# Optimization experiments

Measured on AMD Instinct MI355X. Metric: run time of the kernel, lower is better.

## Reference

```python
import jax, jax.numpy as jnp
import numpy as np

HIDDEN = 1024
HEADS = 16
HEAD_DIM = HIDDEN // HEADS
SCALE = float(np.sqrt(HEAD_DIM))


def setup_inputs() -> dict:
    key = jax.random.key(0)
    ks = jax.random.split(key, 9)
    B, S = 4, 8192
    std = 1.0 / np.sqrt(HIDDEN)
    x = jax.random.normal(ks[0], (B, S, HIDDEN), dtype=jnp.float32)
    Wq = jax.random.normal(ks[1], (HIDDEN, HIDDEN), dtype=jnp.float32) * std
    Wk = jax.random.normal(ks[2], (HIDDEN, HIDDEN), dtype=jnp.float32) * std
    Wv = jax.random.normal(ks[3], (HIDDEN, HIDDEN), dtype=jnp.float32) * std
    Wo = jax.random.normal(ks[4], (HIDDEN, HIDDEN), dtype=jnp.float32) * std
    bq = jax.random.normal(ks[5], (HIDDEN,), dtype=jnp.float32) * std
    bk = jax.random.normal(ks[6], (HIDDEN,), dtype=jnp.float32) * std
    bv = jax.random.normal(ks[7], (HIDDEN,), dtype=jnp.float32) * std
    bo = jax.random.normal(ks[8], (HIDDEN,), dtype=jnp.float32) * std
    return {"x": x, "Wq": Wq, "bq": bq, "Wk": Wk, "bk": bk,
            "Wv": Wv, "bv": bv, "Wo": Wo, "bo": bo}


def reference(x, Wq, bq, Wk, bk, Wv, bv, Wo, bo):
    B, S, E = x.shape
    H, D = HEADS, HEAD_DIM
    # torch nn.Linear: y = x @ W^T + b
    q = (jnp.einsum('bse,fe->bsf', x, Wq) + bq).reshape(B, S, H, D)
    k = (jnp.einsum('bse,fe->bsf', x, Wk) + bk).reshape(B, S, H, D)
    v = (jnp.einsum('bse,fe->bsf', x, Wv) + bv).reshape(B, S, H, D)
    # Faithful to source: NO head transpose, so matmul contracts over head_dim
    # with (B,S) as batch dims -> per-token head-mixing scores [B,S,H,H].
    scores = jnp.einsum('bshd,bsgd->bshg', q, k) / SCALE
    probs = jax.nn.softmax(scores, axis=-1)
    attn = jnp.einsum('bshg,bsgd->bshd', probs, v).reshape(B, S, E)
    return jnp.einsum('bse,fe->bsf', attn, Wo) + bo
```

## Files before the change

kernel.cpp:

```cpp
#include <hip/hip_runtime.h>
#include <hip/hip_bf16.h>
#include <cstdint>
#include <type_traits>

#define GLOBAL_AS __attribute__((address_space(1)))
#define LDS_AS    __attribute__((address_space(3)))

typedef short bf16x8 __attribute__((ext_vector_type(8)));
typedef short short8_t __attribute__((ext_vector_type(8)));
typedef float f32x4  __attribute__((ext_vector_type(4)));

static constexpr int E_DIM = 1024;
static constexpr int HD = 64;
static constexpr int QKV_STRIDE = 3072;
static constexpr int KDIM = 1024;
static constexpr int NTK  = KDIM / 64;
static constexpr int NIT  = NTK / 2;

__device__ __forceinline__ float b2f(short s) {
    union { unsigned u; float f; } x;
    x.u = ((unsigned)(unsigned short)s) << 16;
    return x.f;
}
__device__ __forceinline__ short f2b(float f) {
    union { float f; unsigned u; } x; x.f = f;
    unsigned r = x.u + 0x7FFF + ((x.u >> 16) & 1);
    return (short)(r >> 16);
}

__global__ __launch_bounds__(256) void k_prep(
    const float* __restrict__ x,
    const float* __restrict__ Wq, const float* __restrict__ Wk,
    const float* __restrict__ Wv, const float* __restrict__ Wo,
    const float* __restrict__ bq, const float* __restrict__ bk,
    const float* __restrict__ bv,
    short* __restrict__ xb, short* __restrict__ Wqkvb, short* __restrict__ Wob,
    float* __restrict__ bqkv, int n4x, int n4w)
{
    int i = blockIdx.x * 256 + threadIdx.x;
    const float* src;
    short* dst;
    int j;
    if (i < n4x)                       { src = x;  dst = xb;                  j = i; }
    else if (i < n4x + n4w)            { src = Wq; dst = Wqkvb;               j = i - n4x; }
    else if (i < n4x + 2 * n4w)        { src = Wk; dst = Wqkvb + 4 * n4w;     j = i - n4x - n4w; }
    else if (i < n4x + 3 * n4w)        { src = Wv; dst = Wqkvb + 8 * n4w;     j = i - n4x - 2 * n4w; }
    else if (i < n4x + 4 * n4w)        { src = Wo; dst = Wob;                 j = i - n4x - 3 * n4w; }
    else {
        int b = i - (n4x + 4 * n4w);
        if (b < 768) {
            #pragma unroll
            for (int e = 0; e < 4; ++e) {
                int idx = b * 4 + e;
                float v = (idx < 1024) ? bq[idx] : (idx < 2048 ? bk[idx - 1024] : bv[idx - 2048]);
                bqkv[idx] = v;
            }
        }
        return;
    }
    float4 v = reinterpret_cast<const float4*>(src)[j];
    short4 o;
    o.x = f2b(v.x); o.y = f2b(v.y); o.z = f2b(v.z); o.w = f2b(v.w);
    reinterpret_cast<short4*>(dst)[j] = o;
}

template <typename OutT>
__global__ __launch_bounds__(512, 2) void k_gemm256(
    const short* __restrict__ A,
    const short* __restrict__ Bm,
    const float* __restrict__ bias,
    OutT* __restrict__ C,
    int NT_N, int N)
{
    __shared__ short lds[65536];

    const int tid  = threadIdx.x;
    const int lane = tid & 63;
    const int wv   = tid >> 6;
    const int wr   = wv >> 2;
    const int wc   = wv & 3;
    const int frow = lane & 15;
    const int ks   = lane >> 4;
    const int sw   = frow & 7;
    const int sl0  = ((0 + ks) ^ sw) * 8;
    const int sl1  = ((4 + ks) ^ sw) * 8;

    const int nwg = gridDim.x, nper = nwg >> 3, bid = blockIdx.x;
    const int swz = (bid & 7) * nper + (bid >> 3);
    const int m0  = (swz / NT_N) * 256;
    const int n0  = (swz % NT_N) * 256;

    const int ArdBase = wr * 8192;
    const int BrdBase = 16384 + (wc >> 1) * 8192 + (wc & 1) * 4096;

    const int srow = tid >> 3;
    const int ssl  = ((tid & 7) ^ (srow & 7)) * 8;
    const int sdst = tid * 8;

#define GLD(SRC, DST) __builtin_amdgcn_global_load_lds(                            \
        (const GLOBAL_AS short*)(SRC), (LDS_AS short*)(DST), 16, 0, 0)
#define STAGE_A(BUF, HALF, T) do {                                                 \
    const short* s_ = A + (size_t)(m0 + (HALF) * 128 + srow) * KDIM + (T) * 64 + ssl; \
    short* d_ = &lds[(BUF) * 32768 + (HALF) * 8192 + sdst];                        \
    GLD(s_, d_);  GLD(s_ + (size_t)64 * KDIM, d_ + 4096);                          \
} while (0)
#define STAGE_B(BUF, HALF, T) do {                                                 \
    const short* s_ = Bm + (size_t)(n0 + (HALF) * 128 + srow) * KDIM + (T) * 64 + ssl; \
    short* d_ = &lds[(BUF) * 32768 + 16384 + (HALF) * 8192 + sdst];                \
    GLD(s_, d_);  GLD(s_ + (size_t)64 * KDIM, d_ + 4096);                          \
} while (0)

#define RD_A(BUF, MIB) do {                                                        \
    _Pragma("unroll")                                                              \
    for (int m_ = 0; m_ < 4; ++m_) {                                               \
        const short* p_ = &lds[(BUF) * 32768 + ArdBase + ((MIB) + m_) * 1024 + frow * 64]; \
        af[m_][0] = *(const bf16x8*)(p_ + sl0);                                    \
        af[m_][1] = *(const bf16x8*)(p_ + sl1);                                    \
    }                                                                              \
} while (0)
#define RD_B(BUF, NIB, BF) do {                                                    \
    _Pragma("unroll")                                                              \
    for (int n_ = 0; n_ < 2; ++n_) {                                               \
        const short* p_ = &lds[(BUF) * 32768 + BrdBase + ((NIB) + n_) * 1024 + frow * 64]; \
        BF[n_][0] = *(const bf16x8*)(p_ + sl0);                                    \
        BF[n_][1] = *(const bf16x8*)(p_ + sl1);                                    \
    }                                                                              \
} while (0)

#define MM2(MB) do {                                                               \
    __builtin_amdgcn_s_setprio(1);                                                 \
    _Pragma("unroll")                                                              \
    for (int m_ = 0; m_ < 4; ++m_) {                                               \
        _Pragma("unroll")                                                          \
        for (int n_ = 0; n_ < 2; ++n_) {                                           \
            acc[(MB)+m_][n_] = __builtin_amdgcn_mfma_f32_16x16x32_bf16(            \
                af[m_][0], bfA[n_][0], acc[(MB)+m_][n_], 0, 0, 0);                 \
            acc[(MB)+m_][n_] = __builtin_amdgcn_mfma_f32_16x16x32_bf16(            \
                af[m_][1], bfA[n_][1], acc[(MB)+m_][n_], 0, 0, 0);                 \
            acc[(MB)+m_][2+n_] = __builtin_amdgcn_mfma_f32_16x16x32_bf16(          \
                af[m_][0], bfB[n_][0], acc[(MB)+m_][2+n_], 0, 0, 0);               \
            acc[(MB)+m_][2+n_] = __builtin_amdgcn_mfma_f32_16x16x32_bf16(          \
                af[m_][1], bfB[n_][1], acc[(MB)+m_][2+n_], 0, 0, 0);               \
        }                                                                          \
    }                                                                              \
    __builtin_amdgcn_s_setprio(0);                                                 \
} while (0)

#define BAR   __builtin_amdgcn_s_barrier()
#define VM4   asm volatile("s_waitcnt vmcnt(4)" ::: "memory")
#define VM8   asm volatile("s_waitcnt vmcnt(8)" ::: "memory")

    f32x4 acc[8][4];
    #pragma unroll
    for (int i = 0; i < 8; ++i)
        #pragma unroll
        for (int j = 0; j < 4; ++j)
            acc[i][j] = (f32x4){0.f, 0.f, 0.f, 0.f};

    bf16x8 af[4][2], bfA[2][2], bfB[2][2];

    STAGE_A(0, 0, 0);  STAGE_A(0, 1, 0);  STAGE_B(0, 0, 0);  STAGE_B(0, 1, 0);
    STAGE_A(1, 0, 1);  STAGE_A(1, 1, 1);  STAGE_B(1, 0, 1);  STAGE_B(1, 1, 1);
    VM8;  BAR;
    RD_A(0, 0);  RD_B(0, 0, bfA);  RD_B(0, 2, bfB);

    #pragma unroll 1
    for (int it = 0; it < NIT; ++it) {
        const int tb = (2 * it + 2 <= 15) ? 2 * it + 2 : 15;
        const int tc = (2 * it + 3 <= 15) ? 2 * it + 3 : 15;

        BAR;
        MM2(0);
        RD_A(0, 4);
        STAGE_B(0, 0, tb);  STAGE_B(0, 1, tb);
        VM4;
        BAR;
        MM2(4);
        STAGE_A(0, 0, tb);  STAGE_A(0, 1, tb);
        RD_A(1, 0);  RD_B(1, 0, bfA);  RD_B(1, 2, bfB);
        BAR;
        MM2(0);
        RD_A(1, 4);
        STAGE_B(1, 0, tc);  STAGE_B(1, 1, tc);
        VM4;
        BAR;
        MM2(4);
        STAGE_A(1, 0, tc);  STAGE_A(1, 1, tc);
        RD_A(0, 0);  RD_B(0, 0, bfA);  RD_B(0, 2, bfB);
    }

    asm volatile("s_waitcnt vmcnt(0)" ::: "memory");

    const int crow = (lane >> 4) * 4;
    const int ccol = lane & 15;
    float bv4[4];
    #pragma unroll
    for (int ni = 0; ni < 4; ++ni)
        bv4[ni] = bias[n0 + wc * 64 + ni * 16 + ccol];
    #pragma unroll
    for (int mi = 0; mi < 8; ++mi) {
        #pragma unroll
        for (int r = 0; r < 4; ++r) {
            const size_t rowg = (size_t)(m0 + wr * 128 + mi * 16 + crow + r) * N;
            #pragma unroll
            for (int ni = 0; ni < 4; ++ni) {
                const int col = n0 + wc * 64 + ni * 16 + ccol;
                float v = acc[mi][ni][r] + bv4[ni];
                if constexpr (std::is_same<OutT, float>::value) {
                    C[rowg + col] = v;
                } else {
                    C[rowg + col] = f2b(v);
                }
            }
        }
    }
#undef GLD
#undef STAGE_A
#undef STAGE_B
#undef RD_A
#undef RD_B
#undef MM2
#undef BAR
#undef VM4
#undef VM8
}

__global__ __launch_bounds__(256) void k_attn(
    const short* __restrict__ QKV, short* __restrict__ O)
{
    __shared__ short Ks[16][1032];
    __shared__ short Vs[16][1032];

    const int tid = threadIdx.x;
    const int tok0 = blockIdx.x * 16;

    for (int i = tid; i < 2048; i += 256) {
        int t = i >> 7;
        int j = i & 127;
        const size_t base = (size_t)(tok0 + t) * QKV_STRIDE;
        *reinterpret_cast<short8_t*>(&Ks[t][j * 8]) =
            *reinterpret_cast<const short8_t*>(&QKV[base + 1024 + j * 8]);
        *reinterpret_cast<short8_t*>(&Vs[t][j * 8]) =
            *reinterpret_cast<const short8_t*>(&QKV[base + 2048 + j * 8]);
    }
    __syncthreads();

    const int tl = tid >> 4;
    const int h  = tid & 15;

    float qf[64];
    const short* qp = QKV + (size_t)(tok0 + tl) * QKV_STRIDE + h * HD;
    #pragma unroll
    for (int i = 0; i < 8; ++i) {
        short8_t v = *reinterpret_cast<const short8_t*>(&qp[i * 8]);
        #pragma unroll
        for (int j = 0; j < 8; ++j) qf[i * 8 + j] = b2f(v[j]);
    }

    float s[16];
    #pragma unroll
    for (int g = 0; g < 16; ++g) {
        float a = 0.f;
        #pragma unroll
        for (int i = 0; i < 8; ++i) {
            short8_t kv = *reinterpret_cast<const short8_t*>(&Ks[tl][g * HD + i * 8]);
            #pragma unroll
            for (int j = 0; j < 8; ++j) a += qf[i * 8 + j] * b2f(kv[j]);
        }
        s[g] = a * 0.125f;
    }
    float mx = s[0];
    #pragma unroll
    for (int g = 1; g < 16; ++g) mx = fmaxf(mx, s[g]);
    float l = 0.f;
    #pragma unroll
    for (int g = 0; g < 16; ++g) { s[g] = __expf(s[g] - mx); l += s[g]; }
    const float inv = 1.f / l;
    #pragma unroll
    for (int g = 0; g < 16; ++g) s[g] *= inv;

    short* op = O + (size_t)(tok0 + tl) * E_DIM + h * HD;
    #pragma unroll
    for (int c = 0; c < 4; ++c) {
        float a[16];
        #pragma unroll
        for (int j = 0; j < 16; ++j) a[j] = 0.f;
        #pragma unroll
        for (int g = 0; g < 16; ++g) {
            short8_t v0 = *reinterpret_cast<const short8_t*>(&Vs[tl][g * HD + c * 16]);
            short8_t v1 = *reinterpret_cast<const short8_t*>(&Vs[tl][g * HD + c * 16 + 8]);
            #pragma unroll
            for (int j = 0; j < 8; ++j) {
                a[j]     += s[g] * b2f(v0[j]);
                a[8 + j] += s[g] * b2f(v1[j]);
            }
        }
        short8_t o0, o1;
        #pragma unroll
        for (int j = 0; j < 8; ++j) { o0[j] = f2b(a[j]); o1[j] = f2b(a[8 + j]); }
        *reinterpret_cast<short8_t*>(&op[c * 16])     = o0;
        *reinterpret_cast<short8_t*>(&op[c * 16 + 8]) = o1;
    }
}

extern "C" void kernel_launch(void* const* d_in, const int* in_sizes, int n_in,
                              void* d_out, int out_size, void* d_ws, size_t ws_size,
                              hipStream_t stream) {
    const float* x  = (const float*)d_in[0];
    const float* Wq = (const float*)d_in[1];
    const float* bq = (const float*)d_in[2];
    const float* Wk = (const float*)d_in[3];
    const float* bk = (const float*)d_in[4];
    const float* Wv = (const float*)d_in[5];
    const float* bv = (const float*)d_in[6];
    const float* Wo = (const float*)d_in[7];
    const float* bo = (const float*)d_in[8];
    float* out = (float*)d_out;

    const int T = in_sizes[0] / E_DIM;
    char* ws = (char*)d_ws;
    const size_t SZ_X    = (size_t)T * E_DIM * 2;
    const size_t SZ_WQKV = (size_t)3 * E_DIM * E_DIM * 2;
    const size_t SZ_W    = (size_t)E_DIM * E_DIM * 2;
    const size_t SZ_B    = 3072 * sizeof(float) + 4096;

    short* xb    = (short*)(ws);
    short* Wqkvb = (short*)(ws + SZ_X);
    short* Wob   = (short*)(ws + SZ_X + SZ_WQKV);
    float* bqkv  = (float*)(ws + SZ_X + SZ_WQKV + SZ_W);
    short* QKVb  = (short*)(ws + SZ_X + SZ_WQKV + SZ_W + SZ_B);
    short* Ab    = xb;

    const int n4x = T * E_DIM / 4;
    const int n4w = E_DIM * E_DIM / 4;
    const int nprep = n4x + 4 * n4w + 768;
    k_prep<<<dim3((nprep + 255) / 256), dim3(256), 0, stream>>>(
        x, Wq, Wk, Wv, Wo, bq, bk, bv, xb, Wqkvb, Wob, bqkv, n4x, n4w);

    k_gemm256<short><<<dim3((T / 256) * (QKV_STRIDE / 256)), dim3(512), 0, stream>>>(
        xb, Wqkvb, bqkv, QKVb, QKV_STRIDE / 256, QKV_STRIDE);

    k_attn<<<dim3(T / 16), dim3(256), 0, stream>>>(QKVb, Ab);

    k_gemm256<float><<<dim3((T / 256) * (E_DIM / 256)), dim3(512), 0, stream>>>(
        Ab, Wob, bo, out, E_DIM / 256, E_DIM);
}
```

Before: 393.5 us.

## Use 4-wave 256x256 GEMM blocks with 128x128 per-wave tiles

The GEMM kernel drops from 8 waves to 4 waves per 256x256 block, so each wave computes a 128x128 output tile with 8x8 MFMA accumulators. Global-to-LDS staging issues four loads per thread instead of two, and the wait counts are doubled to match. Each wave now reuses more data per LDS read and there are fewer waves to synchronise, but accumulator register pressure rises sharply (256 floats), which could limit occupancy or cause spills, and there is less latency hiding.

```diff
diff --git a/kernel.cpp b/kernel.cpp
--- a/kernel.cpp
+++ b/kernel.cpp
@@ -65,7 +65,7 @@
 }
 
 template <typename OutT>
-__global__ __launch_bounds__(512, 2) void k_gemm256(
+__global__ __launch_bounds__(256, 1) void k_gemm256(
     const short* __restrict__ A,
     const short* __restrict__ Bm,
     const float* __restrict__ bias,
@@ -77,8 +77,8 @@
     const int tid  = threadIdx.x;
     const int lane = tid & 63;
     const int wv   = tid >> 6;
-    const int wr   = wv >> 2;
-    const int wc   = wv & 3;
+    const int wr   = wv >> 1;
+    const int wc   = wv & 1;
     const int frow = lane & 15;
     const int ks   = lane >> 4;
     const int sw   = frow & 7;
@@ -91,23 +91,26 @@
     const int n0  = (swz % NT_N) * 256;
 
     const int ArdBase = wr * 8192;
-    const int BrdBase = 16384 + (wc >> 1) * 8192 + (wc & 1) * 4096;
+    const int BrdBase = 16384 + wc * 8192;
 
     const int srow = tid >> 3;
     const int ssl  = ((tid & 7) ^ (srow & 7)) * 8;
-    const int sdst = tid * 8;
 
 #define GLD(SRC, DST) __builtin_amdgcn_global_load_lds(                            \
         (const GLOBAL_AS short*)(SRC), (LDS_AS short*)(DST), 16, 0, 0)
 #define STAGE_A(BUF, HALF, T) do {                                                 \
-    const short* s_ = A + (size_t)(m0 + (HALF) * 128 + srow) * KDIM + (T) * 64 + ssl; \
-    short* d_ = &lds[(BUF) * 32768 + (HALF) * 8192 + sdst];                        \
-    GLD(s_, d_);  GLD(s_ + (size_t)64 * KDIM, d_ + 4096);                          \
+    _Pragma("unroll")                                                              \
+    for (int q_ = 0; q_ < 4; ++q_) {                                               \
+        GLD(A + (size_t)(m0 + (HALF) * 128 + srow + 32 * q_) * KDIM + (T) * 64 + ssl, \
+            &lds[(BUF) * 32768 + (HALF) * 8192 + (tid + 256 * q_) * 8]);           \
+    }                                                                              \
 } while (0)
 #define STAGE_B(BUF, HALF, T) do {                                                 \
-    const short* s_ = Bm + (size_t)(n0 + (HALF) * 128 + srow) * KDIM + (T) * 64 + ssl; \
-    short* d_ = &lds[(BUF) * 32768 + 16384 + (HALF) * 8192 + sdst];                \
-    GLD(s_, d_);  GLD(s_ + (size_t)64 * KDIM, d_ + 4096);                          \
+    _Pragma("unroll")                                                              \
+    for (int q_ = 0; q_ < 4; ++q_) {                                               \
+        GLD(Bm + (size_t)(n0 + (HALF) * 128 + srow + 32 * q_) * KDIM + (T) * 64 + ssl, \
+            &lds[(BUF) * 32768 + 16384 + (HALF) * 8192 + (tid + 256 * q_) * 8]);   \
+    }                                                                              \
 } while (0)
 
 #define RD_A(BUF, MIB) do {                                                        \
@@ -120,7 +123,7 @@
 } while (0)
 #define RD_B(BUF, NIB, BF) do {                                                    \
     _Pragma("unroll")                                                              \
-    for (int n_ = 0; n_ < 2; ++n_) {                                               \
+    for (int n_ = 0; n_ < 4; ++n_) {                                               \
         const short* p_ = &lds[(BUF) * 32768 + BrdBase + ((NIB) + n_) * 1024 + frow * 64]; \
         BF[n_][0] = *(const bf16x8*)(p_ + sl0);                                    \
         BF[n_][1] = *(const bf16x8*)(p_ + sl1);                                    \
@@ -132,37 +135,37 @@
     _Pragma("unroll")                                                              \
     for (int m_ = 0; m_ < 4; ++m_) {                                               \
         _Pragma("unroll")                                                          \
-        for (int n_ = 0; n_ < 2; ++n_) {                                           \
+        for (int n_ = 0; n_ < 4; ++n_) {                                           \
             acc[(MB)+m_][n_] = __builtin_amdgcn_mfma_f32_16x16x32_bf16(            \
                 af[m_][0], bfA[n_][0], acc[(MB)+m_][n_], 0, 0, 0);                 \
             acc[(MB)+m_][n_] = __builtin_amdgcn_mfma_f32_16x16x32_bf16(            \
                 af[m_][1], bfA[n_][1], acc[(MB)+m_][n_], 0, 0, 0);                 \
-            acc[(MB)+m_][2+n_] = __builtin_amdgcn_mfma_f32_16x16x32_bf16(          \
-                af[m_][0], bfB[n_][0], acc[(MB)+m_][2+n_], 0, 0, 0);               \
-            acc[(MB)+m_][2+n_] = __builtin_amdgcn_mfma_f32_16x16x32_bf16(          \
-                af[m_][1], bfB[n_][1], acc[(MB)+m_][2+n_], 0, 0, 0);               \
+            acc[(MB)+m_][4+n_] = __builtin_amdgcn_mfma_f32_16x16x32_bf16(          \
+                af[m_][0], bfB[n_][0], acc[(MB)+m_][4+n_], 0, 0, 0);               \
+            acc[(MB)+m_][4+n_] = __builtin_amdgcn_mfma_f32_16x16x32_bf16(          \
+                af[m_][1], bfB[n_][1], acc[(MB)+m_][4+n_], 0, 0, 0);               \
         }                                                                          \
     }                                                                              \
     __builtin_amdgcn_s_setprio(0);                                                 \
 } while (0)
 
 #define BAR   __builtin_amdgcn_s_barrier()
-#define VM4   asm volatile("s_waitcnt vmcnt(4)" ::: "memory")
 #define VM8   asm volatile("s_waitcnt vmcnt(8)" ::: "memory")
-
-    f32x4 acc[8][4];
+#define VM16  asm volatile("s_waitcnt vmcnt(16)" ::: "memory")
+
+    f32x4 acc[8][8];
     #pragma unroll
     for (int i = 0; i < 8; ++i)
         #pragma unroll
-        for (int j = 0; j < 4; ++j)
+        for (int j = 0; j < 8; ++j)
             acc[i][j] = (f32x4){0.f, 0.f, 0.f, 0.f};
 
-    bf16x8 af[4][2], bfA[2][2], bfB[2][2];
+    bf16x8 af[4][2], bfA[4][2], bfB[4][2];
 
     STAGE_A(0, 0, 0);  STAGE_A(0, 1, 0);  STAGE_B(0, 0, 0);  STAGE_B(0, 1, 0);
     STAGE_A(1, 0, 1);  STAGE_A(1, 1, 1);  STAGE_B(1, 0, 1);  STAGE_B(1, 1, 1);
-    VM8;  BAR;
-    RD_A(0, 0);  RD_B(0, 0, bfA);  RD_B(0, 2, bfB);
+    VM16;  BAR;
+    RD_A(0, 0);  RD_B(0, 0, bfA);  RD_B(0, 4, bfB);
 
     #pragma unroll 1
     for (int it = 0; it < NIT; ++it) {
@@ -173,39 +176,39 @@
         MM2(0);
         RD_A(0, 4);
         STAGE_B(0, 0, tb);  STAGE_B(0, 1, tb);
-        VM4;
+        VM8;
         BAR;
         MM2(4);
         STAGE_A(0, 0, tb);  STAGE_A(0, 1, tb);
-        RD_A(1, 0);  RD_B(1, 0, bfA);  RD_B(1, 2, bfB);
+        RD_A(1, 0);  RD_B(1, 0, bfA);  RD_B(1, 4, bfB);
         BAR;
         MM2(0);
         RD_A(1, 4);
         STAGE_B(1, 0, tc);  STAGE_B(1, 1, tc);
-        VM4;
+        VM8;
         BAR;
         MM2(4);
         STAGE_A(1, 0, tc);  STAGE_A(1, 1, tc);
-        RD_A(0, 0);  RD_B(0, 0, bfA);  RD_B(0, 2, bfB);
+        RD_A(0, 0);  RD_B(0, 0, bfA);  RD_B(0, 4, bfB);
     }
 
     asm volatile("s_waitcnt vmcnt(0)" ::: "memory");
 
     const int crow = (lane >> 4) * 4;
     const int ccol = lane & 15;
-    float bv4[4];
-    #pragma unroll
-    for (int ni = 0; ni < 4; ++ni)
-        bv4[ni] = bias[n0 + wc * 64 + ni * 16 + ccol];
+    float bv8[8];
+    #pragma unroll
+    for (int ni = 0; ni < 8; ++ni)
+        bv8[ni] = bias[n0 + wc * 128 + ni * 16 + ccol];
     #pragma unroll
     for (int mi = 0; mi < 8; ++mi) {
         #pragma unroll
         for (int r = 0; r < 4; ++r) {
             const size_t rowg = (size_t)(m0 + wr * 128 + mi * 16 + crow + r) * N;
             #pragma unroll
-            for (int ni = 0; ni < 4; ++ni) {
-                const int col = n0 + wc * 64 + ni * 16 + ccol;
-                float v = acc[mi][ni][r] + bv4[ni];
+            for (int ni = 0; ni < 8; ++ni) {
+                const int col = n0 + wc * 128 + ni * 16 + ccol;
+                float v = acc[mi][ni][r] + bv8[ni];
                 if constexpr (std::is_same<OutT, float>::value) {
                     C[rowg + col] = v;
                 } else {
@@ -221,8 +224,8 @@
 #undef RD_B
 #undef MM2
 #undef BAR
-#undef VM4
 #undef VM8
+#undef VM16
 }
 
 __global__ __launch_bounds__(256) void k_attn(
@@ -337,11 +340,11 @@
     k_prep<<<dim3((nprep + 255) / 256), dim3(256), 0, stream>>>(
         x, Wq, Wk, Wv, Wo, bq, bk, bv, xb, Wqkvb, Wob, bqkv, n4x, n4w);
 
-    k_gemm256<short><<<dim3((T / 256) * (QKV_STRIDE / 256)), dim3(512), 0, stream>>>(
+    k_gemm256<short><<<dim3((T / 256) * (QKV_STRIDE / 256)), dim3(256), 0, stream>>>(
         xb, Wqkvb, bqkv, QKVb, QKV_STRIDE / 256, QKV_STRIDE);
 
     k_attn<<<dim3(T / 16), dim3(256), 0, stream>>>(QKVb, Ab);
 
-    k_gemm256<float><<<dim3((T / 256) * (E_DIM / 256)), dim3(512), 0, stream>>>(
+    k_gemm256<float><<<dim3((T / 256) * (E_DIM / 256)), dim3(256), 0, stream>>>(
         Ab, Wob, bo, out, E_DIM / 256, E_DIM);
 }
```

New measurement: 1.091 ms. 177% more time.
